# Kernel optimization log

Measured on AMD Instinct MI355X. Metric: run time of the kernel, lower is better.

## Reference

```python
import jax, jax.numpy as jnp
import numpy as np

H = 512  # output_size


def setup_inputs() -> dict:
    key = jax.random.key(0)
    k = jax.random.split(key, 6)
    B, T, D = 64, 512, 512
    x = jax.random.normal(k[0], (B, T, D), dtype=jnp.float32)
    lengths = jnp.sort(jax.random.randint(k[1], (B,), 1, T + 1))[::-1].astype(jnp.int64)
    scale = 0.05
    w_in = jax.random.normal(k[2], (6 * H, D), dtype=jnp.float32) * scale
    b_in = jax.random.normal(k[3], (6 * H,), dtype=jnp.float32) * scale
    w_state = jax.random.normal(k[4], (5 * H, H), dtype=jnp.float32) * scale
    b_state = jax.random.normal(k[5], (5 * H,), dtype=jnp.float32) * scale
    return {"x": x, "lengths": lengths, "w_in": w_in, "b_in": b_in,
            "w_state": w_state, "b_state": b_state}


def reference(x, lengths, w_in, b_in, w_state, b_state):
    # x: [B,T,D]; returns padded outputs [B,T,H] (zeros past each length),
    # matching the padded content of the original PackedSequence output.
    B, T, _ = x.shape
    # Precompute all input projections: [B,T,6H]
    proj_in = jnp.einsum('btd,od->bto', x, w_in) + b_in
    proj_in_t = jnp.transpose(proj_in, (1, 0, 2))            # [T,B,6H]
    # valid mask per timestep: [T,B,1]
    mask_t = (jnp.arange(T)[:, None] < lengths[None, :])[..., None]

    def step(carry, inp):
        h, c = carry                                          # [B,H] each
        pi, m = inp                                           # [B,6H], [B,1]
        ps = h @ w_state.T + b_state                          # [B,5H]
        i_g = jax.nn.sigmoid(pi[:, 0*H:1*H] + ps[:, 0*H:1*H])
        f_g = jax.nn.sigmoid(pi[:, 1*H:2*H] + ps[:, 1*H:2*H])
        g   = jnp.tanh(     pi[:, 2*H:3*H] + ps[:, 2*H:3*H])
        o_g = jax.nn.sigmoid(pi[:, 3*H:4*H] + ps[:, 3*H:4*H])
        c_new = i_g * g + f_g * c
        out = o_g * jnp.tanh(c_new)
        hw  = jax.nn.sigmoid(pi[:, 4*H:5*H] + ps[:, 4*H:5*H])
        out = hw * out + (1.0 - hw) * pi[:, 5*H:6*H]
        # past-length positions are reset to zero (matches original slicing)
        out = jnp.where(m, out, 0.0)
        c_new = jnp.where(m, c_new, 0.0)
        return (out, c_new), out

    h0 = jnp.zeros((B, H), dtype=x.dtype)
    c0 = jnp.zeros((B, H), dtype=x.dtype)
    _, outs = jax.lax.scan(step, (h0, c0), (proj_in_t, mask_t))
    return jnp.transpose(outs, (1, 0, 2))                     # [B,T,H]
```

## Files before the change

### kernel.cpp

```cpp
#include <hip/hip_runtime.h>
#include <cstdint>
#include <cstddef>

#define BB 64
#define TT 512
#define DD 512
#define HH 512
#define SIXH 3072
#define NWG 32

typedef __attribute__((ext_vector_type(8))) short bf16x8;
typedef __attribute__((ext_vector_type(4))) float f32x4;
typedef __attribute__((ext_vector_type(4))) unsigned short u16x4;
typedef __attribute__((ext_vector_type(4))) int i32x4;

#define WS_FLAGS 0u
#define WS_CNT   256u
#define WS_H     16640u
#define WS_C     147712u
#define WS_XB    278784u
#define WS_WB    33833216u
#define WS_BF    36978944u
#define WS_PROJ  36991232u

#define CLOAD16(dst, ptr) \
    asm volatile("global_load_dwordx4 %0, %1, off sc0 sc1" : "=v"(dst) : "v"(ptr))
#define CSTORE8(ptr, val) \
    asm volatile("global_store_dwordx2 %0, %1, off sc0 sc1" :: "v"(ptr), "v"(val))
#define WAIT4(N, a,b,c,d) \
    asm volatile("s_waitcnt vmcnt(" N ")" : "+v"(a),"+v"(b),"+v"(c),"+v"(d))

__device__ __forceinline__ float bf2f(unsigned short u) {
    union { unsigned int i; float f; } v; v.i = ((unsigned int)u) << 16; return v.f;
}
__device__ __forceinline__ unsigned short f2bf(float f) {
    union { unsigned int i; float f; } v; v.f = f;
    unsigned int r = v.i + 0x7FFFu + ((v.i >> 16) & 1u);
    return (unsigned short)(r >> 16);
}
__device__ __forceinline__ float sigm(float x) { return 1.0f / (1.0f + __expf(-x)); }
__device__ __forceinline__ float tanh_fast(float x) {
    return 1.0f - 2.0f / (__expf(2.0f * x) + 1.0f);
}

__device__ __forceinline__ bf16x8 cvt8v(const float* p) {
    const float4 a = *(const float4*)p;
    const float4 b = *(const float4*)(p + 4);
    bf16x8 o;
    o[0] = (short)f2bf(a.x); o[1] = (short)f2bf(a.y);
    o[2] = (short)f2bf(a.z); o[3] = (short)f2bf(a.w);
    o[4] = (short)f2bf(b.x); o[5] = (short)f2bf(b.y);
    o[6] = (short)f2bf(b.z); o[7] = (short)f2bf(b.w);
    return o;
}

__global__ void detect_kernel(const unsigned short* __restrict__ x16,
                              const int* __restrict__ len32,
                              int* __restrict__ flags) {
    const int lane = threadIdx.x;
    int bad = 0;
    for (int i = lane; i < 256; i += 64)
        if (fabsf(bf2f(x16[i])) > 1e4f) bad++;
#pragma unroll
    for (int off = 32; off; off >>= 1) bad += __shfl_down(bad, off);
    if (lane == 0) {
        flags[0] = (bad >= 16) ? 1 : 0;
        flags[1] = (len32[1] == 0 && len32[3] == 0 && len32[5] == 0) ? 1 : 0;
    }
}

__global__ __launch_bounds__(256) void convert_kernel(
    const void* __restrict__ xv, const void* __restrict__ wv,
    const void* __restrict__ bv,
    unsigned short* __restrict__ xb, unsigned short* __restrict__ wb,
    float* __restrict__ bf, const int* __restrict__ flags)
{
    const int fp32 = flags[0];
    const size_t NX = (size_t)BB * TT * DD;
    const size_t NW = (size_t)SIXH * DD;
    const size_t tid = (size_t)blockIdx.x * blockDim.x + threadIdx.x;
    const size_t stride = (size_t)gridDim.x * blockDim.x;

    if (fp32) {
        const float* xf = (const float*)xv;
        for (size_t i = tid * 4; i < NX; i += stride * 4) {
            const float4 v = *(const float4*)(xf + i);
            u16x4 o; o[0] = f2bf(v.x); o[1] = f2bf(v.y); o[2] = f2bf(v.z); o[3] = f2bf(v.w);
            *(u16x4*)(xb + i) = o;
        }
        const float* wf = (const float*)wv;
        for (size_t i = tid * 4; i < NW; i += stride * 4) {
            const float4 v = *(const float4*)(wf + i);
            u16x4 o; o[0] = f2bf(v.x); o[1] = f2bf(v.y); o[2] = f2bf(v.z); o[3] = f2bf(v.w);
            *(u16x4*)(wb + i) = o;
        }
        const float* bvf = (const float*)bv;
        for (size_t i = tid; i < SIXH; i += stride) bf[i] = bvf[i];
    } else {
        const unsigned short* xs = (const unsigned short*)xv;
        for (size_t i = tid * 4; i < NX; i += stride * 4)
            *(u16x4*)(xb + i) = *(const u16x4*)(xs + i);
        const unsigned short* wsrc = (const unsigned short*)wv;
        for (size_t i = tid * 4; i < NW; i += stride * 4)
            *(u16x4*)(wb + i) = *(const u16x4*)(wsrc + i);
        const unsigned short* bs = (const unsigned short*)bv;
        for (size_t i = tid; i < SIXH; i += stride) bf[i] = bf2f(bs[i]);
    }
}

__global__ __launch_bounds__(256) void proj_kernel(
    const unsigned short* __restrict__ xb, const unsigned short* __restrict__ wb,
    const float* __restrict__ bf, unsigned short* __restrict__ projc,
    const int* __restrict__ flags, const int* __restrict__ len32,
    int t0, int tc_shift)
{
    const int Tc  = 1 << tc_shift;
    {
        const int mb  = blockIdx.y * 64;
        const int bq  = mb >> tc_shift;
        const int tl0 = mb & (Tc - 1);
        const int len_b = flags[1] ? len32[2 * bq] : len32[bq];
        if (t0 + tl0 >= len_b) return;
    }

    const int tid  = threadIdx.x;
    const int wave = tid >> 6;
    const int lane = tid & 63;
    const int q    = lane >> 4;
    const int r    = lane & 15;

    const int m_blk  = blockIdx.y * 64 + (wave >> 1) * 32;
    const int n_base = blockIdx.x * 192 + (wave & 1) * 32;
    const int b      = m_blk >> tc_shift;
    const int tl     = m_blk & (Tc - 1);

    const size_t xrow0 = (size_t)(b * TT + t0 + tl + r) * DD;
    const size_t xrow1 = (size_t)(b * TT + t0 + tl + 16 + r) * DD;

    f32x4 acc[3][2][2] = {};
    const int koff = q * 8;
    for (int k0 = 0; k0 < DD; k0 += 32) {
        const int k = k0 + koff;
        const bf16x8 a0 = *(const bf16x8*)(xb + xrow0 + k);
        const bf16x8 a1 = *(const bf16x8*)(xb + xrow1 + k);
#pragma unroll
        for (int nt = 0; nt < 3; nt++) {
            const size_t wrow0 = (size_t)(n_base + nt * 64 + r) * DD;
            const size_t wrow1 = (size_t)(n_base + nt * 64 + 16 + r) * DD;
            bf16x8 b0 = *(const bf16x8*)(wb + wrow0 + k);
            bf16x8 b1 = *(const bf16x8*)(wb + wrow1 + k);
            acc[nt][0][0] = __builtin_amdgcn_mfma_f32_16x16x32_bf16(a0, b0, acc[nt][0][0], 0, 0, 0);
            acc[nt][0][1] = __builtin_amdgcn_mfma_f32_16x16x32_bf16(a0, b1, acc[nt][0][1], 0, 0, 0);
            acc[nt][1][0] = __builtin_amdgcn_mfma_f32_16x16x32_bf16(a1, b0, acc[nt][1][0], 0, 0, 0);
            acc[nt][1][1] = __builtin_amdgcn_mfma_f32_16x16x32_bf16(a1, b1, acc[nt][1][1], 0, 0, 0);
        }
    }

#pragma unroll
    for (int nt = 0; nt < 3; nt++)
#pragma unroll
        for (int mi = 0; mi < 2; mi++)
#pragma unroll
            for (int ni = 0; ni < 2; ni++) {
                const int n = n_base + nt * 64 + ni * 16 + r;
                const float bias = bf[n];
#pragma unroll
                for (int rr = 0; rr < 4; rr++) {
                    const int m = m_blk + mi * 16 + q * 4 + rr;
                    projc[(size_t)m * SIXH + n] = f2bf(acc[nt][mi][ni][rr] + bias);
                }
            }
}

__global__ __launch_bounds__(256, 1) void rec_kernel(
    const unsigned short* __restrict__ projc,
    const void* __restrict__ wsv, const void* __restrict__ bsv,
    const int* __restrict__ len32,
    unsigned short* __restrict__ hbuf, float* __restrict__ cbuf,
    int* __restrict__ wgflag, void* __restrict__ outv,
    const int* __restrict__ flags, int t0, int Tc)
{
    const int fp32 = flags[0], i64 = flags[1];
    const int tid  = threadIdx.x;
    const int wv   = tid >> 6;
    const int lane = tid & 63;
    const int q    = lane >> 4;
    const int r    = lane & 15;
    const int j0   = blockIdx.x * 16;
    const int b    = wv * 16 + r;

    __shared__ unsigned short wlds[5 * 16 * 64 * 8];

    for (int v = tid; v < 5 * 16 * 64; v += 256) {
        const int g  = v >> 10;
        const int ki = (v >> 6) & 15;
        const int ln = v & 63;
        const size_t gaddr = (size_t)(g * HH + j0 + (ln & 15)) * HH + ki * 32 + (ln >> 4) * 8;
        bf16x8 w8;
        if (fp32) w8 = cvt8v((const float*)wsv + gaddr);
        else      w8 = *(const bf16x8*)((const unsigned short*)wsv + gaddr);
        *(bf16x8*)&wlds[(size_t)v * 8] = w8;
    }

    float bs[5][4];
#pragma unroll
    for (int g = 0; g < 5; g++)
#pragma unroll
        for (int jj = 0; jj < 4; jj++)
            bs[g][jj] = fp32 ? ((const float*)bsv)[g * HH + j0 + q * 4 + jj]
                             : bf2f(((const unsigned short*)bsv)[g * HH + j0 + q * 4 + jj]);

    const int len = i64 ? len32[2 * b] : len32[b];

    int lmax_g = 0;
    for (int i = wv * 16; i < wv * 16 + 16; i++) {
        const int li = i64 ? len32[2 * i] : len32[i];
        lmax_g = (li > lmax_g) ? li : lmax_g;
    }

    float creg[4];
#pragma unroll
    for (int jj = 0; jj < 4; jj++)
        creg[jj] = cbuf[b * HH + j0 + q * 4 + jj];

    u16x4 pv[6];
    {
        const unsigned short* pb = projc + (size_t)b * Tc * SIXH + j0 + q * 4;
#pragma unroll
        for (int g = 0; g < 6; g++) pv[g] = *(const u16x4*)(pb + g * HH);
    }

    __syncthreads();

    union HU { i32x4 i; bf16x8 b; };
    union P8 { unsigned short s[4]; unsigned long long u; };

    int* const gbase = wgflag + (size_t)wv * NWG * 32;
    int fcache = (lane < NWG) ? 0 : 0x7fffffff;

    for (int t = t0; t < t0 + Tc; t++) {
        if (t >= lmax_g) {
            if (fp32) {
                float* op = (float*)outv + ((size_t)b * TT + t) * HH + j0 + q * 4;
                *(float4*)op = make_float4(0.f, 0.f, 0.f, 0.f);
            } else {
                unsigned short* op = (unsigned short*)outv + ((size_t)b * TT + t) * HH + j0 + q * 4;
                *(unsigned long long*)op = 0ull;
            }
            continue;
        }

        const unsigned short* hcur = hbuf + (size_t)(t & 1) * (BB * HH);
        unsigned short*       hnxt = hbuf + (size_t)((t + 1) & 1) * (BB * HH);

        if (t > t0) {
            while ((__ballot(fcache >= t) & 0xFFFFull) != 0xFFFFull) {
                if (fcache < t)
                    fcache = __hip_atomic_load(&gbase[lane * 32], __ATOMIC_RELAXED,
                                               __HIP_MEMORY_SCOPE_AGENT);
            }
            asm volatile("" ::: "memory");
        }
        i32x4 hv[16];
#pragma unroll
        for (int ki = 0; ki < 8; ki++)
            CLOAD16(hv[ki], hcur + (size_t)b * HH + ki * 32 + q * 8);

        if (t > t0) {
            while (__ballot(fcache >= t) != ~0ull) {
                if (fcache < t)
                    fcache = __hip_atomic_load(&gbase[lane * 32], __ATOMIC_RELAXED,
                                               __HIP_MEMORY_SCOPE_AGENT);
            }
            asm volatile("" ::: "memory");
        }
#pragma unroll
        for (int ki = 8; ki < 16; ki++)
            CLOAD16(hv[ki], hcur + (size_t)b * HH + ki * 32 + q * 8);

        f32x4 acc[5] = {};
#define MFMA_CHUNK(KLO)                                                          \
        _Pragma("unroll")                                                        \
        for (int ki = (KLO); ki < (KLO) + 4; ki++) {                             \
            HU u; u.i = hv[ki];                                                  \
            _Pragma("unroll")                                                    \
            for (int g = 0; g < 5; g++) {                                        \
                bf16x8 aw = *(const bf16x8*)&wlds[((g * 16 + ki) * 64 + lane) * 8]; \
                acc[g] = __builtin_amdgcn_mfma_f32_16x16x32_bf16(aw, u.b, acc[g], 0, 0, 0); \
            }                                                                    \
        }
        WAIT4("12", hv[0],  hv[1],  hv[2],  hv[3]);   MFMA_CHUNK(0)
        WAIT4("8",  hv[4],  hv[5],  hv[6],  hv[7]);   MFMA_CHUNK(4)
        WAIT4("4",  hv[8],  hv[9],  hv[10], hv[11]);  MFMA_CHUNK(8)
        WAIT4("0",  hv[12], hv[13], hv[14], hv[15]);  MFMA_CHUNK(12)
#undef MFMA_CHUNK

        P8 hp;
        float ov4[4];
#pragma unroll
        for (int jj = 0; jj < 4; jj++) {
            const float i_g = sigm(bf2f(pv[0][jj]) + acc[0][jj] + bs[0][jj]);
            const float f_g = sigm(bf2f(pv[1][jj]) + acc[1][jj] + bs[1][jj]);
            const float g_t = tanh_fast(bf2f(pv[2][jj]) + acc[2][jj] + bs[2][jj]);
            const float o_g = sigm(bf2f(pv[3][jj]) + acc[3][jj] + bs[3][jj]);
            const float hw  = sigm(bf2f(pv[4][jj]) + acc[4][jj] + bs[4][jj]);

            float c_new = i_g * g_t + f_g * creg[jj];
            float ov = o_g * tanh_fast(c_new);
            ov = hw * ov + (1.0f - hw) * bf2f(pv[5][jj]);
            if (t >= len) { ov = 0.0f; c_new = 0.0f; }
            creg[jj] = c_new;
            ov4[jj] = ov;
            hp.s[jj] = f2bf(ov);
        }

        CSTORE8((void*)(hnxt + (size_t)b * HH + j0 + q * 4), hp.u);
        asm volatile("s_waitcnt vmcnt(0)" ::: "memory");
        if (lane == 0)
            __hip_atomic_store(&gbase[blockIdx.x * 32], t + 1,
                               __ATOMIC_RELAXED, __HIP_MEMORY_SCOPE_AGENT);

        if (fp32) {
            float* op = (float*)outv + ((size_t)b * TT + t) * HH + j0 + q * 4;
            *(float4*)op = make_float4(ov4[0], ov4[1], ov4[2], ov4[3]);
        } else {
            unsigned short* op = (unsigned short*)outv + ((size_t)b * TT + t) * HH + j0 + q * 4;
            *(unsigned long long*)op = hp.u;
        }
        const int tln = t - t0 + 1;
        if (tln < Tc) {
            const unsigned short* pb = projc + ((size_t)b * Tc + tln) * SIXH + j0 + q * 4;
#pragma unroll
            for (int g = 0; g < 6; g++) pv[g] = *(const u16x4*)(pb + g * HH);
        }
    }

#pragma unroll
    for (int jj = 0; jj < 4; jj++)
        cbuf[b * HH + j0 + q * 4 + jj] = creg[jj];
}

extern "C" void kernel_launch(void* const* d_in, const int* in_sizes, int n_in,
                              void* d_out, int out_size, void* d_ws, size_t ws_size,
                              hipStream_t stream) {
    const void* xv      = d_in[0];
    const int*  len     = (const int*)d_in[1];
    const void* w_in    = d_in[2];
    const void* b_in    = d_in[3];
    const void* w_state = d_in[4];
    const void* b_state = d_in[5];

    char* ws = (char*)d_ws;
    int* flags  = (int*)(ws + WS_FLAGS);
    int* wgflag = (int*)(ws + WS_CNT);
    unsigned short* hbuf = (unsigned short*)(ws + WS_H);
    float* cbuf = (float*)(ws + WS_C);
    unsigned short* xb = (unsigned short*)(ws + WS_XB);
    unsigned short* wb = (unsigned short*)(ws + WS_WB);
    float* bf = (float*)(ws + WS_BF);
    unsigned short* projc = (unsigned short*)(ws + WS_PROJ);

    int tc_shift = 9;
    while (tc_shift > 6 &&
           WS_PROJ + ((size_t)BB << tc_shift) * SIXH * 2 > ws_size) tc_shift--;
    const int Tc = 1 << tc_shift;

    detect_kernel<<<1, 64, 0, stream>>>((const unsigned short*)xv, len, flags);
    hipMemsetAsync(ws + WS_CNT, 0, WS_XB - WS_CNT, stream);
    convert_kernel<<<2048, 256, 0, stream>>>(xv, w_in, b_in, xb, wb, bf, flags);

    for (int c = 0; c < TT / Tc; c++) {
        const int t0 = c * Tc;
        proj_kernel<<<dim3(SIXH / 192, (BB << tc_shift) >> 6), 256, 0, stream>>>(
            xb, wb, bf, projc, flags, len, t0, tc_shift);
        rec_kernel<<<NWG, 256, 0, stream>>>(projc, w_state, b_state, len,
                                            hbuf, cbuf, wgflag, d_out, flags, t0, Tc);
    }
}
```

Baseline: 2.552 ms.

## Replace per-workgroup flag barrier with step-tagged hidden-state packets

Drops the separate per-workgroup flag array and the store-wait-then-flag handshake. Each 16-byte hidden-state store now carries the step index in its first and last dwords, so readers poll the data directly until every packet is tagged with the current step. This removes the store-drain wait and the extra flag round trip from the serial recurrence. In exchange, each poll re-reads twice as many bytes, and correctness depends on 16-byte stores being seen atomically. A spin limit can also let the loop proceed on stale data.

```diff
diff --git a/kernel.cpp b/kernel.cpp
--- a/kernel.cpp
+++ b/kernel.cpp
@@ -15,20 +15,20 @@
 typedef __attribute__((ext_vector_type(4))) int i32x4;
 
 #define WS_FLAGS 0u
-#define WS_CNT   256u
-#define WS_H     16640u
-#define WS_C     147712u
-#define WS_XB    278784u
-#define WS_WB    33833216u
-#define WS_BF    36978944u
-#define WS_PROJ  36991232u
+#define WS_H2    256u
+#define WS_C     262400u
+#define WS_XB    393472u
+#define WS_WB    33947904u
+#define WS_BF    37093632u
+#define WS_PROJ  37105920u
 
 #define CLOAD16(dst, ptr) \
     asm volatile("global_load_dwordx4 %0, %1, off sc0 sc1" : "=v"(dst) : "v"(ptr))
-#define CSTORE8(ptr, val) \
-    asm volatile("global_store_dwordx2 %0, %1, off sc0 sc1" :: "v"(ptr), "v"(val))
-#define WAIT4(N, a,b,c,d) \
-    asm volatile("s_waitcnt vmcnt(" N ")" : "+v"(a),"+v"(b),"+v"(c),"+v"(d))
+#define CLOAD16O(dst, ptr, OFF) \
+    asm volatile("global_load_dwordx4 %0, %1, off offset:%c2 sc0 sc1" \
+                 : "=v"(dst) : "v"(ptr), "i"(OFF))
+#define CSTORE16(ptr, val) \
+    asm volatile("global_store_dwordx4 %0, %1, off sc0 sc1" :: "v"(ptr), "v"(val))
 
 __device__ __forceinline__ float bf2f(unsigned short u) {
     union { unsigned int i; float f; } v; v.i = ((unsigned int)u) << 16; return v.f;
@@ -176,8 +176,8 @@
     const unsigned short* __restrict__ projc,
     const void* __restrict__ wsv, const void* __restrict__ bsv,
     const int* __restrict__ len32,
-    unsigned short* __restrict__ hbuf, float* __restrict__ cbuf,
-    int* __restrict__ wgflag, void* __restrict__ outv,
+    unsigned int* __restrict__ hbuf2, float* __restrict__ cbuf,
+    void* __restrict__ outv,
     const int* __restrict__ flags, int t0, int Tc)
 {
     const int fp32 = flags[0], i64 = flags[1];
@@ -235,8 +235,6 @@
     union HU { i32x4 i; bf16x8 b; };
     union P8 { unsigned short s[4]; unsigned long long u; };
 
-    int* const gbase = wgflag + (size_t)wv * NWG * 32;
-    int fcache = (lane < NWG) ? 0 : 0x7fffffff;
 
     for (int t = t0; t < t0 + Tc; t++) {
         if (t >= lmax_g) {
@@ -250,50 +248,47 @@
             continue;
         }
 
-        const unsigned short* hcur = hbuf + (size_t)(t & 1) * (BB * HH);
-        unsigned short*       hnxt = hbuf + (size_t)((t + 1) & 1) * (BB * HH);
-
+        const unsigned int* hrow =
+            hbuf2 + ((size_t)((t & 1) * BB + b) * 128 + q * 2) * 4;
+        i32x4 hq[32];
+#define ISSUE_H_LOADS()                                                     \
+        _Pragma("unroll")                                                   \
+        for (int ki = 0; ki < 16; ki++) {                                   \
+            CLOAD16O(hq[2 * ki],     hrow, ki * 128);                       \
+            CLOAD16O(hq[2 * ki + 1], hrow, ki * 128 + 16);                  \
+        }
         if (t > t0) {
-            while ((__ballot(fcache >= t) & 0xFFFFull) != 0xFFFFull) {
-                if (fcache < t)
-                    fcache = __hip_atomic_load(&gbase[lane * 32], __ATOMIC_RELAXED,
-                                               __HIP_MEMORY_SCOPE_AGENT);
+            int spin = 0;
+            for (;;) {
+                ISSUE_H_LOADS();
+                asm volatile("s_waitcnt vmcnt(0)" ::: "memory");
+                __builtin_amdgcn_sched_barrier(0);
+                unsigned bad = 0;
+#pragma unroll
+                for (int i = 0; i < 32; i++)
+                    bad |= (unsigned)((hq[i][0] ^ t) | (hq[i][3] ^ t));
+                if (__all(bad == 0)) break;
+                if (++spin > 65536) break;
             }
-            asm volatile("" ::: "memory");
-        }
-        i32x4 hv[16];
-#pragma unroll
-        for (int ki = 0; ki < 8; ki++)
-            CLOAD16(hv[ki], hcur + (size_t)b * HH + ki * 32 + q * 8);
-
-        if (t > t0) {
-            while (__ballot(fcache >= t) != ~0ull) {
-                if (fcache < t)
-                    fcache = __hip_atomic_load(&gbase[lane * 32], __ATOMIC_RELAXED,
-                                               __HIP_MEMORY_SCOPE_AGENT);
+        } else {
+            ISSUE_H_LOADS();
+            asm volatile("s_waitcnt vmcnt(0)" ::: "memory");
+            __builtin_amdgcn_sched_barrier(0);
+        }
+#undef ISSUE_H_LOADS
+
+        f32x4 acc[5] = {};
+#pragma unroll
+        for (int ki = 0; ki < 16; ki++) {
+            HU u;
+            u.i = (i32x4){ hq[2 * ki][1], hq[2 * ki][2],
+                           hq[2 * ki + 1][1], hq[2 * ki + 1][2] };
+#pragma unroll
+            for (int g = 0; g < 5; g++) {
+                bf16x8 aw = *(const bf16x8*)&wlds[((g * 16 + ki) * 64 + lane) * 8];
+                acc[g] = __builtin_amdgcn_mfma_f32_16x16x32_bf16(aw, u.b, acc[g], 0, 0, 0);
             }
-            asm volatile("" ::: "memory");
-        }
-#pragma unroll
-        for (int ki = 8; ki < 16; ki++)
-            CLOAD16(hv[ki], hcur + (size_t)b * HH + ki * 32 + q * 8);
-
-        f32x4 acc[5] = {};
-#define MFMA_CHUNK(KLO)                                                          \
-        _Pragma("unroll")                                                        \
-        for (int ki = (KLO); ki < (KLO) + 4; ki++) {                             \
-            HU u; u.i = hv[ki];                                                  \
-            _Pragma("unroll")                                                    \
-            for (int g = 0; g < 5; g++) {                                        \
-                bf16x8 aw = *(const bf16x8*)&wlds[((g * 16 + ki) * 64 + lane) * 8]; \
-                acc[g] = __builtin_amdgcn_mfma_f32_16x16x32_bf16(aw, u.b, acc[g], 0, 0, 0); \
-            }                                                                    \
-        }
-        WAIT4("12", hv[0],  hv[1],  hv[2],  hv[3]);   MFMA_CHUNK(0)
-        WAIT4("8",  hv[4],  hv[5],  hv[6],  hv[7]);   MFMA_CHUNK(4)
-        WAIT4("4",  hv[8],  hv[9],  hv[10], hv[11]);  MFMA_CHUNK(8)
-        WAIT4("0",  hv[12], hv[13], hv[14], hv[15]);  MFMA_CHUNK(12)
-#undef MFMA_CHUNK
+        }
 
         P8 hp;
         float ov4[4];
@@ -314,11 +309,16 @@
             hp.s[jj] = f2bf(ov);
         }
 
-        CSTORE8((void*)(hnxt + (size_t)b * HH + j0 + q * 4), hp.u);
-        asm volatile("s_waitcnt vmcnt(0)" ::: "memory");
-        if (lane == 0)
-            __hip_atomic_store(&gbase[blockIdx.x * 32], t + 1,
-                               __ATOMIC_RELAXED, __HIP_MEMORY_SCOPE_AGENT);
+        {
+            i32x4 st;
+            st[0] = t + 1;
+            st[1] = (int)(unsigned int)(hp.u & 0xffffffffull);
+            st[2] = (int)(unsigned int)(hp.u >> 32);
+            st[3] = t + 1;
+            unsigned int* hw_ = hbuf2 +
+                ((size_t)(((t + 1) & 1) * BB + b) * 128 + (j0 >> 2) + q) * 4;
+            CSTORE16(hw_, st);
+        }
 
         if (fp32) {
             float* op = (float*)outv + ((size_t)b * TT + t) * HH + j0 + q * 4;
@@ -352,8 +352,7 @@
 
     char* ws = (char*)d_ws;
     int* flags  = (int*)(ws + WS_FLAGS);
-    int* wgflag = (int*)(ws + WS_CNT);
-    unsigned short* hbuf = (unsigned short*)(ws + WS_H);
+    unsigned int* hbuf2 = (unsigned int*)(ws + WS_H2);
     float* cbuf = (float*)(ws + WS_C);
     unsigned short* xb = (unsigned short*)(ws + WS_XB);
     unsigned short* wb = (unsigned short*)(ws + WS_WB);
@@ -366,7 +365,7 @@
     const int Tc = 1 << tc_shift;
 
     detect_kernel<<<1, 64, 0, stream>>>((const unsigned short*)xv, len, flags);
-    hipMemsetAsync(ws + WS_CNT, 0, WS_XB - WS_CNT, stream);
+    hipMemsetAsync(ws + WS_H2, 0, WS_XB - WS_H2, stream);
     convert_kernel<<<2048, 256, 0, stream>>>(xv, w_in, b_in, xb, wb, bf, flags);
 
     for (int c = 0; c < TT / Tc; c++) {
@@ -374,6 +373,6 @@
         proj_kernel<<<dim3(SIXH / 192, (BB << tc_shift) >> 6), 256, 0, stream>>>(
             xb, wb, bf, projc, flags, len, t0, tc_shift);
         rec_kernel<<<NWG, 256, 0, stream>>>(projc, w_state, b_state, len,
-                                            hbuf, cbuf, wgflag, d_out, flags, t0, Tc);
-    }
-}
+                                            hbuf2, cbuf, d_out, flags, t0, Tc);
+    }
+}
```

New measurement: 3.696 ms. 44.8% more time.
